# Performance work log

Measured on AMD Instinct MI355X. Metric: run time of the kernel, lower is better.

Reference implementation:

```python
import jax, jax.numpy as jnp
import numpy as np

N_ATOMS = 32768
N_SPECIES = 4
N_FEAT = 7584
HIDDEN = 256
N_STRUCT = 1024


def setup_inputs() -> dict:
    key = jax.random.key(0)
    ks = jax.random.split(key, 12)
    s = 1.0 / np.sqrt(N_FEAT)
    h = 1.0 / np.sqrt(HIDDEN)
    return {
        "features": jax.random.normal(ks[0], (N_ATOMS, N_FEAT), dtype=jnp.float32),
        "structure_index": jax.random.randint(ks[1], (N_ATOMS,), 0, N_STRUCT),
        "n_structures": N_STRUCT,
        "W1": jax.random.normal(ks[2], (N_SPECIES, N_FEAT, HIDDEN), dtype=jnp.float32) * s,
        "b1": jax.random.normal(ks[3], (N_SPECIES, HIDDEN), dtype=jnp.float32) * s,
        "W2": jax.random.normal(ks[4], (N_SPECIES, HIDDEN, HIDDEN), dtype=jnp.float32) * h,
        "b2": jax.random.normal(ks[5], (N_SPECIES, HIDDEN), dtype=jnp.float32) * h,
        "W3": jax.random.normal(ks[6], (N_SPECIES, HIDDEN, HIDDEN), dtype=jnp.float32) * h,
        "b3": jax.random.normal(ks[7], (N_SPECIES, HIDDEN), dtype=jnp.float32) * h,
        "W4": jax.random.normal(ks[8], (N_SPECIES, HIDDEN), dtype=jnp.float32) * h,
        "b4": jax.random.normal(ks[9], (N_SPECIES,), dtype=jnp.float32) * h,
    }


def reference(features, structure_index, n_structures, W1, b1, W2, b2, W3, b3, W4, b4):
    # Atoms are stored as contiguous per-species blocks (as in the equistore
    # TensorMap), so the species-gated gather is a reshape: [S, A, F].
    S = W1.shape[0]
    x = features.reshape(S, -1, features.shape[-1])
    # Per-species 4-layer MLP (grouped GEMMs).
    hdn = jax.nn.silu(jnp.einsum("saf,sfh->sah", x, W1) + b1[:, None, :])
    hdn = jax.nn.silu(jnp.einsum("sah,shk->sak", hdn, W2) + b2[:, None, :])
    hdn = jax.nn.silu(jnp.einsum("sah,shk->sak", hdn, W3) + b3[:, None, :])
    atomic_energies = (jnp.einsum("sah,sh->sa", hdn, W4) + b4[:, None]).reshape(-1)
    # Scatter-add atomic energies into per-structure energies (index_add_).
    energies = jax.ops.segment_sum(atomic_energies, structure_index,
                                   num_segments=n_structures)
    return energies
```

## Files before the change

### kernel.cpp

```cpp
#include <hip/hip_runtime.h>
#include <hip/hip_bf16.h>

#define N_ATOMS   32768
#define N_SPECIES 4
#define N_FEAT    7584
#define HIDDEN    256
#define N_STRUCT  1024
#define APS       8192

typedef __attribute__((ext_vector_type(8))) short bf16x8;
typedef __attribute__((ext_vector_type(4))) float f32x4;

typedef const __attribute__((address_space(1))) void* gptr_t;
typedef __attribute__((address_space(3))) void* lptr_t;

__device__ __forceinline__ unsigned short f2bf(float x) {
    union { float f; unsigned u; } v; v.f = x;
    unsigned r = v.u + 0x7FFFu + ((v.u >> 16) & 1u);
    return (unsigned short)(r >> 16);
}
__device__ __forceinline__ float bf2f(unsigned short h) {
    union { unsigned u; float f; } v; v.u = ((unsigned)h) << 16;
    return v.f;
}

__global__ void transpose_cvt(const float* __restrict__ in,
                              unsigned short* __restrict__ out,
                              int K, int N) {
    __shared__ unsigned short sh[32][33];
    const int s  = blockIdx.z;
    const int k0 = blockIdx.x * 32;
    const int n0 = blockIdx.y * 32;
    const int tx = threadIdx.x & 31;
    const int ty = threadIdx.x >> 5;
    const float* ip = in + (size_t)s * K * N;
    unsigned short* op = out + (size_t)s * N * K;
#pragma unroll
    for (int i = 0; i < 4; ++i) {
        int k = ty + 8 * i;
        sh[tx][k] = f2bf(ip[(size_t)(k0 + k) * N + n0 + tx]);
    }
    __syncthreads();
#pragma unroll
    for (int i = 0; i < 4; ++i) {
        int n = ty + 8 * i;
        op[(size_t)(n0 + n) * K + k0 + tx] = sh[n][tx];
    }
}

template <bool AF32>
__global__ __launch_bounds__(256, 2) void mlp_gemm(
    const void* __restrict__ Ag,
    const unsigned short* __restrict__ Wt,
    const float* __restrict__ bias,
    unsigned short* __restrict__ Out,
    int K) {
    __shared__ unsigned short Asm[64 * 48];
    __shared__ unsigned short Bsm[256 * 32];

    const int tid  = threadIdx.x;
    const int w    = tid >> 6;
    const int lane = tid & 63;
    const int s    = blockIdx.y;
    const int m0   = blockIdx.x * 64;

    const unsigned short* Wts = Wt + (size_t)s * 256 * K;
    const int brow = lane >> 2;
    const int bkin = (lane & 3) * 8;
    const int lm   = lane & 15;
    const int kgl  = (lane >> 4) * 8;
    constexpr int ASTRIDE = AF32 ? 48 : 32;

    f32x4 acc[4][4];
#pragma unroll
    for (int i = 0; i < 4; ++i)
#pragma unroll
        for (int j = 0; j < 4; ++j)
#pragma unroll
            for (int e = 0; e < 4; ++e) acc[i][j][e] = 0.0f;

    for (int k0 = 0; k0 < K; k0 += 32) {
        __syncthreads();

#pragma unroll
        for (int j = 0; j < 4; ++j) {
            const unsigned short* gp =
                Wts + (size_t)(16 * (4 * w + j) + brow) * K + k0 + bkin;
            __builtin_amdgcn_global_load_lds((gptr_t)gp,
                                             (lptr_t)&Bsm[(4 * w + j) * 512],
                                             16, 0, 0);
        }

        if constexpr (AF32) {
            const float* Af = (const float*)Ag + ((size_t)s * APS + m0) * K;
#pragma unroll
            for (int r = 0; r < 2; ++r) {
                int f   = tid + 256 * r;
                int row = f >> 3;
                int c4  = f & 7;
                float4 v = *(const float4*)(Af + (size_t)row * K + k0 + c4 * 4);
                ushort4 b;
                b.x = f2bf(v.x); b.y = f2bf(v.y); b.z = f2bf(v.z); b.w = f2bf(v.w);
                *(ushort4*)(&Asm[row * 48 + c4 * 4]) = b;
            }
        } else {
            const unsigned short* Ab =
                (const unsigned short*)Ag + ((size_t)s * APS + m0) * K;
            const unsigned short* gp = Ab + (size_t)(16 * w + brow) * K + k0 + bkin;
            __builtin_amdgcn_global_load_lds((gptr_t)gp, (lptr_t)&Asm[w * 512],
                                             16, 0, 0);
        }

        __syncthreads();

        bf16x8 af[4], bf[4];
#pragma unroll
        for (int mf = 0; mf < 4; ++mf)
            af[mf] = *(const bf16x8*)(&Asm[(mf * 16 + lm) * ASTRIDE + kgl]);
#pragma unroll
        for (int nf = 0; nf < 4; ++nf)
            bf[nf] = *(const bf16x8*)(&Bsm[(w * 64 + nf * 16 + lm) * 32 + kgl]);
#pragma unroll
        for (int mf = 0; mf < 4; ++mf)
#pragma unroll
            for (int nf = 0; nf < 4; ++nf)
                acc[mf][nf] = __builtin_amdgcn_mfma_f32_16x16x32_bf16(
                    af[mf], bf[nf], acc[mf][nf], 0, 0, 0);
    }

    unsigned short* op = Out + ((size_t)s * APS + m0) * 256;
    const float* bp = bias + s * 256;
    const int q = lane >> 4;
#pragma unroll
    for (int nf = 0; nf < 4; ++nf) {
        int col  = w * 64 + nf * 16 + lm;
        float bv = bp[col];
#pragma unroll
        for (int mf = 0; mf < 4; ++mf)
#pragma unroll
            for (int i = 0; i < 4; ++i) {
                int row = mf * 16 + q * 4 + i;
                float x = acc[mf][nf][i] + bv;
                float y = x / (1.0f + __expf(-x));
                op[(size_t)row * 256 + col] = f2bf(y);
            }
    }
}

__global__ void final_reduce(const unsigned short* __restrict__ H3,
                             const float* __restrict__ W4,
                             const float* __restrict__ b4,
                             const int* __restrict__ sidx,
                             float* __restrict__ out) {
    const int atom = blockIdx.x * 4 + (threadIdx.x >> 6);
    const int lane = threadIdx.x & 63;
    const int s    = atom >> 13;
    ushort4 hv = *(const ushort4*)(H3 + (size_t)atom * 256 + lane * 4);
    float4  wv = *(const float4*)(W4 + s * 256 + lane * 4);
    float sum = bf2f(hv.x) * wv.x + bf2f(hv.y) * wv.y +
                bf2f(hv.z) * wv.z + bf2f(hv.w) * wv.w;
#pragma unroll
    for (int off = 32; off > 0; off >>= 1) sum += __shfl_down(sum, off, 64);
    if (lane == 0) atomicAdd(&out[sidx[atom]], sum + b4[s]);
}

extern "C" void kernel_launch(void* const* d_in, const int* in_sizes, int n_in,
                              void* d_out, int out_size, void* d_ws, size_t ws_size,
                              hipStream_t stream) {
    const float* features = (const float*)d_in[0];
    const int*   sidx     = (const int*)d_in[1];
    const float* W1 = (const float*)d_in[3];
    const float* b1 = (const float*)d_in[4];
    const float* W2 = (const float*)d_in[5];
    const float* b2 = (const float*)d_in[6];
    const float* W3 = (const float*)d_in[7];
    const float* b3 = (const float*)d_in[8];
    const float* W4 = (const float*)d_in[9];
    const float* b4 = (const float*)d_in[10];
    float* out = (float*)d_out;

    char* ws = (char*)d_ws;
    unsigned short* Wt1 = (unsigned short*)ws; ws += (size_t)N_SPECIES * HIDDEN * N_FEAT * 2;
    unsigned short* Wt2 = (unsigned short*)ws; ws += (size_t)N_SPECIES * HIDDEN * HIDDEN * 2;
    unsigned short* Wt3 = (unsigned short*)ws; ws += (size_t)N_SPECIES * HIDDEN * HIDDEN * 2;
    unsigned short* H1  = (unsigned short*)ws; ws += (size_t)N_ATOMS * HIDDEN * 2;
    unsigned short* H2  = (unsigned short*)ws; ws += (size_t)N_ATOMS * HIDDEN * 2;
    unsigned short* H3  = H1;

    hipMemsetAsync(d_out, 0, N_STRUCT * sizeof(float), stream);

    transpose_cvt<<<dim3(N_FEAT / 32, HIDDEN / 32, N_SPECIES), 256, 0, stream>>>(W1, Wt1, N_FEAT, HIDDEN);
    transpose_cvt<<<dim3(HIDDEN / 32, HIDDEN / 32, N_SPECIES), 256, 0, stream>>>(W2, Wt2, HIDDEN, HIDDEN);
    transpose_cvt<<<dim3(HIDDEN / 32, HIDDEN / 32, N_SPECIES), 256, 0, stream>>>(W3, Wt3, HIDDEN, HIDDEN);

    mlp_gemm<true><<<dim3(APS / 64, N_SPECIES), 256, 0, stream>>>(features, Wt1, b1, H1, N_FEAT);
    mlp_gemm<false><<<dim3(APS / 64, N_SPECIES), 256, 0, stream>>>(H1, Wt2, b2, H2, HIDDEN);
    mlp_gemm<false><<<dim3(APS / 64, N_SPECIES), 256, 0, stream>>>(H2, Wt3, b3, H3, HIDDEN);

    final_reduce<<<N_ATOMS / 4, 256, 0, stream>>>(H3, W4, b4, sidx, out);
}
```

Baseline: 1.455 ms.

## Fuse all MLP layers and reduction into one kernel with double-buffered loads

Replaces the three per-layer GEMM launches and the final reduce kernel with a single fused kernel. Hidden activations for a 64-atom tile stay in shared memory between layers, and the W4 dot product plus atomic scatter happen at the end. The layer-1 K loop gains double buffering: the next A tile is prefetched into registers and the next B tile into a second LDS buffer while MFMAs run on the current one. This removes the global round trips for the intermediate activations and the extra launches. In exchange LDS use rises to roughly 75 KB per block, which may cut occupancy below the declared two blocks per CU.

```diff
diff --git a/kernel.cpp b/kernel.cpp
--- a/kernel.cpp
+++ b/kernel.cpp
@@ -48,120 +48,196 @@
     }
 }
 
-template <bool AF32>
-__global__ __launch_bounds__(256, 2) void mlp_gemm(
-    const void* __restrict__ Ag,
-    const unsigned short* __restrict__ Wt,
-    const float* __restrict__ bias,
-    unsigned short* __restrict__ Out,
-    int K) {
-    __shared__ unsigned short Asm[64 * 48];
-    __shared__ unsigned short Bsm[256 * 32];
+
+__device__ __forceinline__ void stage_B(const unsigned short* __restrict__ Wts,
+                                        int K, int k0,
+                                        unsigned short* BsmBuf, int w, int lane) {
+#pragma unroll
+    for (int j = 0; j < 4; ++j) {
+        const unsigned short* gp =
+            Wts + (size_t)(16 * (4 * w + j) + (lane >> 2)) * K + k0 + (lane & 3) * 8;
+        __builtin_amdgcn_global_load_lds((gptr_t)gp,
+                                         (lptr_t)&BsmBuf[(4 * w + j) * 512],
+                                         16, 0, 0);
+    }
+}
+
+__device__ __forceinline__ void load_A(const float* __restrict__ Af, int K, int k0,
+                                       int tid, float4 v[2]) {
+#pragma unroll
+    for (int r = 0; r < 2; ++r) {
+        int f = tid + 256 * r;
+        int row = f >> 3, c4 = f & 7;
+        v[r] = *(const float4*)(Af + (size_t)row * K + k0 + c4 * 4);
+    }
+}
+__device__ __forceinline__ void commit_A(unsigned short* AsmBuf, int tid,
+                                         const float4 v[2]) {
+#pragma unroll
+    for (int r = 0; r < 2; ++r) {
+        int f = tid + 256 * r;
+        int row = f >> 3, c4 = f & 7;
+        ushort4 b;
+        b.x = f2bf(v[r].x); b.y = f2bf(v[r].y);
+        b.z = f2bf(v[r].z); b.w = f2bf(v[r].w);
+        *(ushort4*)(&AsmBuf[row * 48 + c4 * 4]) = b;
+    }
+}
+
+#define HPAD 264
+
+__global__ __launch_bounds__(256, 2) void fused_mlp(
+    const float* __restrict__ features,
+    const unsigned short* __restrict__ Wt1,
+    const float* __restrict__ b1,
+    const unsigned short* __restrict__ Wt2,
+    const float* __restrict__ b2,
+    const unsigned short* __restrict__ Wt3,
+    const float* __restrict__ b3,
+    const float* __restrict__ W4,
+    const float* __restrict__ b4,
+    const int* __restrict__ sidx,
+    float* __restrict__ out) {
+    __shared__ unsigned short Asm[2][64 * 48];
+    __shared__ unsigned short Bsm[2][256 * 32];
+    __shared__ unsigned short Hsm[64 * HPAD];
 
     const int tid  = threadIdx.x;
     const int w    = tid >> 6;
     const int lane = tid & 63;
-    const int s    = blockIdx.y;
-    const int m0   = blockIdx.x * 64;
-
-    const unsigned short* Wts = Wt + (size_t)s * 256 * K;
-    const int brow = lane >> 2;
-    const int bkin = (lane & 3) * 8;
     const int lm   = lane & 15;
-    const int kgl  = (lane >> 4) * 8;
-    constexpr int ASTRIDE = AF32 ? 48 : 32;
+    const int q    = lane >> 4;
+    const int kgl  = q * 8;
+    const int s    = blockIdx.x >> 7;
+    const int m0   = (blockIdx.x & 127) * 64;
 
     f32x4 acc[4][4];
-#pragma unroll
-    for (int i = 0; i < 4; ++i)
-#pragma unroll
-        for (int j = 0; j < 4; ++j)
-#pragma unroll
-            for (int e = 0; e < 4; ++e) acc[i][j][e] = 0.0f;
-
-    for (int k0 = 0; k0 < K; k0 += 32) {
+
+    {
+        const float* Af = features + ((size_t)s * APS + m0) * N_FEAT;
+        const unsigned short* Wts = Wt1 + (size_t)s * 256 * N_FEAT;
+#pragma unroll
+        for (int i = 0; i < 4; ++i)
+#pragma unroll
+            for (int j = 0; j < 4; ++j)
+#pragma unroll
+                for (int e = 0; e < 4; ++e) acc[i][j][e] = 0.0f;
+
+        float4 av[2];
+        stage_B(Wts, N_FEAT, 0, Bsm[0], w, lane);
+        load_A(Af, N_FEAT, 0, tid, av);
+        commit_A(Asm[0], tid, av);
+
+        int buf = 0;
+        for (int k0 = 0; k0 < N_FEAT; k0 += 32, buf ^= 1) {
+            __syncthreads();
+            const bool more = (k0 + 32 < N_FEAT);
+            if (more) {
+                stage_B(Wts, N_FEAT, k0 + 32, Bsm[buf ^ 1], w, lane);
+                load_A(Af, N_FEAT, k0 + 32, tid, av);
+            }
+            bf16x8 af[4], bfr[4];
+#pragma unroll
+            for (int mf = 0; mf < 4; ++mf)
+                af[mf] = *(const bf16x8*)(&Asm[buf][(mf * 16 + lm) * 48 + kgl]);
+#pragma unroll
+            for (int nf = 0; nf < 4; ++nf)
+                bfr[nf] = *(const bf16x8*)(&Bsm[buf][(w * 64 + nf * 16 + lm) * 32 + kgl]);
+#pragma unroll
+            for (int mf = 0; mf < 4; ++mf)
+#pragma unroll
+                for (int nf = 0; nf < 4; ++nf)
+                    acc[mf][nf] = __builtin_amdgcn_mfma_f32_16x16x32_bf16(
+                        af[mf], bfr[nf], acc[mf][nf], 0, 0, 0);
+            if (more) commit_A(Asm[buf ^ 1], tid, av);
+        }
         __syncthreads();
-
-#pragma unroll
-        for (int j = 0; j < 4; ++j) {
-            const unsigned short* gp =
-                Wts + (size_t)(16 * (4 * w + j) + brow) * K + k0 + bkin;
-            __builtin_amdgcn_global_load_lds((gptr_t)gp,
-                                             (lptr_t)&Bsm[(4 * w + j) * 512],
-                                             16, 0, 0);
-        }
-
-        if constexpr (AF32) {
-            const float* Af = (const float*)Ag + ((size_t)s * APS + m0) * K;
-#pragma unroll
-            for (int r = 0; r < 2; ++r) {
-                int f   = tid + 256 * r;
-                int row = f >> 3;
-                int c4  = f & 7;
-                float4 v = *(const float4*)(Af + (size_t)row * K + k0 + c4 * 4);
-                ushort4 b;
-                b.x = f2bf(v.x); b.y = f2bf(v.y); b.z = f2bf(v.z); b.w = f2bf(v.w);
-                *(ushort4*)(&Asm[row * 48 + c4 * 4]) = b;
-            }
-        } else {
-            const unsigned short* Ab =
-                (const unsigned short*)Ag + ((size_t)s * APS + m0) * K;
-            const unsigned short* gp = Ab + (size_t)(16 * w + brow) * K + k0 + bkin;
-            __builtin_amdgcn_global_load_lds((gptr_t)gp, (lptr_t)&Asm[w * 512],
-                                             16, 0, 0);
-        }
-
+        const float* bp = b1 + s * 256;
+#pragma unroll
+        for (int nf = 0; nf < 4; ++nf) {
+            int col = w * 64 + nf * 16 + lm;
+            float bv = bp[col];
+#pragma unroll
+            for (int mf = 0; mf < 4; ++mf)
+#pragma unroll
+                for (int i = 0; i < 4; ++i) {
+                    int row = mf * 16 + q * 4 + i;
+                    float x = acc[mf][nf][i] + bv;
+                    Hsm[row * HPAD + col] = f2bf(x / (1.0f + __expf(-x)));
+                }
+        }
+    }
+
+#pragma unroll 1
+    for (int layer = 0; layer < 2; ++layer) {
+        const unsigned short* Wts =
+            (layer == 0 ? Wt2 : Wt3) + (size_t)s * 256 * 256;
+        const float* bp = (layer == 0 ? b2 : b3) + s * 256;
+#pragma unroll
+        for (int i = 0; i < 4; ++i)
+#pragma unroll
+            for (int j = 0; j < 4; ++j)
+#pragma unroll
+                for (int e = 0; e < 4; ++e) acc[i][j][e] = 0.0f;
+
+        stage_B(Wts, 256, 0, Bsm[0], w, lane);
+        int buf = 0;
+        for (int k0 = 0; k0 < 256; k0 += 32, buf ^= 1) {
+            __syncthreads();
+            if (k0 + 32 < 256)
+                stage_B(Wts, 256, k0 + 32, Bsm[buf ^ 1], w, lane);
+            bf16x8 af[4], bfr[4];
+#pragma unroll
+            for (int mf = 0; mf < 4; ++mf)
+                af[mf] = *(const bf16x8*)(&Hsm[(mf * 16 + lm) * HPAD + k0 + kgl]);
+#pragma unroll
+            for (int nf = 0; nf < 4; ++nf)
+                bfr[nf] = *(const bf16x8*)(&Bsm[buf][(w * 64 + nf * 16 + lm) * 32 + kgl]);
+#pragma unroll
+            for (int mf = 0; mf < 4; ++mf)
+#pragma unroll
+                for (int nf = 0; nf < 4; ++nf)
+                    acc[mf][nf] = __builtin_amdgcn_mfma_f32_16x16x32_bf16(
+                        af[mf], bfr[nf], acc[mf][nf], 0, 0, 0);
+        }
         __syncthreads();
-
-        bf16x8 af[4], bf[4];
-#pragma unroll
-        for (int mf = 0; mf < 4; ++mf)
-            af[mf] = *(const bf16x8*)(&Asm[(mf * 16 + lm) * ASTRIDE + kgl]);
-#pragma unroll
-        for (int nf = 0; nf < 4; ++nf)
-            bf[nf] = *(const bf16x8*)(&Bsm[(w * 64 + nf * 16 + lm) * 32 + kgl]);
-#pragma unroll
-        for (int mf = 0; mf < 4; ++mf)
-#pragma unroll
-            for (int nf = 0; nf < 4; ++nf)
-                acc[mf][nf] = __builtin_amdgcn_mfma_f32_16x16x32_bf16(
-                    af[mf], bf[nf], acc[mf][nf], 0, 0, 0);
-    }
-
-    unsigned short* op = Out + ((size_t)s * APS + m0) * 256;
-    const float* bp = bias + s * 256;
-    const int q = lane >> 4;
-#pragma unroll
-    for (int nf = 0; nf < 4; ++nf) {
-        int col  = w * 64 + nf * 16 + lm;
-        float bv = bp[col];
-#pragma unroll
-        for (int mf = 0; mf < 4; ++mf)
-#pragma unroll
-            for (int i = 0; i < 4; ++i) {
-                int row = mf * 16 + q * 4 + i;
-                float x = acc[mf][nf][i] + bv;
-                float y = x / (1.0f + __expf(-x));
-                op[(size_t)row * 256 + col] = f2bf(y);
-            }
-    }
-}
-
-__global__ void final_reduce(const unsigned short* __restrict__ H3,
-                             const float* __restrict__ W4,
-                             const float* __restrict__ b4,
-                             const int* __restrict__ sidx,
-                             float* __restrict__ out) {
-    const int atom = blockIdx.x * 4 + (threadIdx.x >> 6);
-    const int lane = threadIdx.x & 63;
-    const int s    = atom >> 13;
-    ushort4 hv = *(const ushort4*)(H3 + (size_t)atom * 256 + lane * 4);
-    float4  wv = *(const float4*)(W4 + s * 256 + lane * 4);
-    float sum = bf2f(hv.x) * wv.x + bf2f(hv.y) * wv.y +
-                bf2f(hv.z) * wv.z + bf2f(hv.w) * wv.w;
-#pragma unroll
-    for (int off = 32; off > 0; off >>= 1) sum += __shfl_down(sum, off, 64);
-    if (lane == 0) atomicAdd(&out[sidx[atom]], sum + b4[s]);
+#pragma unroll
+        for (int nf = 0; nf < 4; ++nf) {
+            int col = w * 64 + nf * 16 + lm;
+            float bv = bp[col];
+#pragma unroll
+            for (int mf = 0; mf < 4; ++mf)
+#pragma unroll
+                for (int i = 0; i < 4; ++i) {
+                    int row = mf * 16 + q * 4 + i;
+                    float x = acc[mf][nf][i] + bv;
+                    Hsm[row * HPAD + col] = f2bf(x / (1.0f + __expf(-x)));
+                }
+        }
+    }
+
+    __syncthreads();
+    {
+        const float* W4s = W4 + s * 256;
+        const int a_loc = w * 16 + lm;
+        float sum = 0.0f;
+#pragma unroll
+        for (int j8 = 0; j8 < 8; ++j8) {
+            bf16x8 hv = *(const bf16x8*)(&Hsm[a_loc * HPAD + q * 64 + j8 * 8]);
+            float4 w0 = *(const float4*)(W4s + q * 64 + j8 * 8);
+            float4 w1 = *(const float4*)(W4s + q * 64 + j8 * 8 + 4);
+            sum += bf2f((unsigned short)hv[0]) * w0.x + bf2f((unsigned short)hv[1]) * w0.y +
+                   bf2f((unsigned short)hv[2]) * w0.z + bf2f((unsigned short)hv[3]) * w0.w +
+                   bf2f((unsigned short)hv[4]) * w1.x + bf2f((unsigned short)hv[5]) * w1.y +
+                   bf2f((unsigned short)hv[6]) * w1.z + bf2f((unsigned short)hv[7]) * w1.w;
+        }
+        sum += __shfl_xor(sum, 16, 64);
+        sum += __shfl_xor(sum, 32, 64);
+        if (q == 0) {
+            int atom = s * APS + m0 + a_loc;
+            atomicAdd(&out[sidx[atom]], sum + b4[s]);
+        }
+    }
 }
 
 extern "C" void kernel_launch(void* const* d_in, const int* in_sizes, int n_in,
@@ -183,9 +259,6 @@
     unsigned short* Wt1 = (unsigned short*)ws; ws += (size_t)N_SPECIES * HIDDEN * N_FEAT * 2;
     unsigned short* Wt2 = (unsigned short*)ws; ws += (size_t)N_SPECIES * HIDDEN * HIDDEN * 2;
     unsigned short* Wt3 = (unsigned short*)ws; ws += (size_t)N_SPECIES * HIDDEN * HIDDEN * 2;
-    unsigned short* H1  = (unsigned short*)ws; ws += (size_t)N_ATOMS * HIDDEN * 2;
-    unsigned short* H2  = (unsigned short*)ws; ws += (size_t)N_ATOMS * HIDDEN * 2;
-    unsigned short* H3  = H1;
 
     hipMemsetAsync(d_out, 0, N_STRUCT * sizeof(float), stream);
 
@@ -193,9 +266,6 @@
     transpose_cvt<<<dim3(HIDDEN / 32, HIDDEN / 32, N_SPECIES), 256, 0, stream>>>(W2, Wt2, HIDDEN, HIDDEN);
     transpose_cvt<<<dim3(HIDDEN / 32, HIDDEN / 32, N_SPECIES), 256, 0, stream>>>(W3, Wt3, HIDDEN, HIDDEN);
 
-    mlp_gemm<true><<<dim3(APS / 64, N_SPECIES), 256, 0, stream>>>(features, Wt1, b1, H1, N_FEAT);
-    mlp_gemm<false><<<dim3(APS / 64, N_SPECIES), 256, 0, stream>>>(H1, Wt2, b2, H2, HIDDEN);
-    mlp_gemm<false><<<dim3(APS / 64, N_SPECIES), 256, 0, stream>>>(H2, Wt3, b3, H3, HIDDEN);
-
-    final_reduce<<<N_ATOMS / 4, 256, 0, stream>>>(H3, W4, b4, sidx, out);
-}
+    fused_mlp<<<dim3(N_ATOMS / 64), 256, 0, stream>>>(
+        features, Wt1, b1, Wt2, b2, Wt3, b3, W4, b4, sidx, out);
+}
```

New measurement: 1.440 ms. Within noise of the previous version (-1.0%).
